# Kernel tuning notes

Measured on AMD Instinct MI355X. Metric: run time of the kernel, lower is better.

The kernel has to match this reference:

```python
import jax, jax.numpy as jnp
import numpy as np

BATCH = 4096
FEAT = 1024
HID = 1024


def setup_inputs() -> dict:
    key = jax.random.key(0)
    ks = jax.random.split(key, 11)
    s_x = 1.0 / np.sqrt(FEAT)
    s_h = 1.0 / np.sqrt(HID)
    return {
        "x": jax.random.normal(ks[0], (BATCH, FEAT), jnp.float32),
        "h_prev": jax.random.normal(ks[1], (BATCH, HID), jnp.float32),
        "c_prev": jax.random.normal(ks[2], (BATCH, HID), jnp.float32),
        # Dense(3*hidden) on x and h (keras Dense: y = x @ W + b)
        "W_ifo_x": jax.random.normal(ks[3], (FEAT, 3 * HID), jnp.float32) * s_x,
        "b_ifo_x": jnp.zeros((3 * HID,), jnp.float32),
        "W_ifo_h": jax.random.normal(ks[4], (HID, 3 * HID), jnp.float32) * s_h,
        "b_ifo_h": jnp.zeros((3 * HID,), jnp.float32),
        # Dense(hidden) on x and h for candidate 'a'
        "W_b_x": jax.random.normal(ks[5], (FEAT, HID), jnp.float32) * s_x,
        "b_b_x": jnp.zeros((HID,), jnp.float32),
        "W_b_h": jax.random.normal(ks[6], (HID, HID), jnp.float32) * s_h,
        "b_b_h": jnp.zeros((HID,), jnp.float32),
    }


def reference(x, h_prev, c_prev, W_ifo_x, b_ifo_x, W_ifo_h, b_ifo_h,
              W_b_x, b_b_x, W_b_h, b_b_h):
    # Fused gate projections: [B, 3H]
    ifo = jax.nn.sigmoid(x @ W_ifo_x + b_ifo_x + h_prev @ W_ifo_h + b_ifo_h)
    i, f, o = jnp.split(ifo, 3, axis=-1)
    a = jnp.tanh(x @ W_b_x + b_b_x + h_prev @ W_b_h + b_b_h)
    c = i * a + f * c_prev
    h = o * jnp.tanh(c)
    return (h, c)
```

## Files before the change

kernel.cpp:

```cpp
#include <hip/hip_runtime.h>
#include <hip/hip_bf16.h>
#include <stdint.h>
#include <stddef.h>


#define BATCH 4096
#define FEAT  1024
#define HID   1024
#define NCAT  4096
#define KCAT  2048

typedef __attribute__((ext_vector_type(8)))  __bf16 bf16x8;
typedef __attribute__((ext_vector_type(16))) float  floatx16;

__device__ __forceinline__ unsigned short f2bf(float f) {
    __hip_bfloat16 b = __float2bfloat16(f);
    return *reinterpret_cast<unsigned short*>(&b);
}
__device__ __forceinline__ void gl2lds16(const unsigned short* g, unsigned short* l) {
    __builtin_amdgcn_global_load_lds(
        (const __attribute__((address_space(1))) void*)g,
        (__attribute__((address_space(3))) void*)l, 16, 0, 0);
}

#define TP_PAD 72
__global__ __launch_bounds__(256)
void pack_all(const float* __restrict__ x, const float* __restrict__ h,
              const float* __restrict__ Wix, const float* __restrict__ Wih,
              const float* __restrict__ Wbx, const float* __restrict__ Wbh,
              unsigned short* __restrict__ Xcat, unsigned short* __restrict__ Wt) {
    __shared__ unsigned short tile[64 * TP_PAD];
    const int t = threadIdx.x;
    const int b = blockIdx.x;
    if (b >= 2048) {
        const int rb = (b - 2048) * 8;
#pragma unroll
        for (int it = 0; it < 8; ++it) {
            const int m = rb + it;
            const float* src = (t < 128) ? (x + (size_t)m * FEAT + t * 8)
                                         : (h + (size_t)m * HID + (t - 128) * 8);
            float4 v0 = *(const float4*)src;
            float4 v1 = *(const float4*)(src + 4);
            union { unsigned short s16[8]; uint4 v; } pk;
            pk.s16[0] = f2bf(v0.x); pk.s16[1] = f2bf(v0.y);
            pk.s16[2] = f2bf(v0.z); pk.s16[3] = f2bf(v0.w);
            pk.s16[4] = f2bf(v1.x); pk.s16[5] = f2bf(v1.y);
            pk.s16[6] = f2bf(v1.z); pk.s16[7] = f2bf(v1.w);
            *(uint4*)(Xcat + (size_t)m * KCAT + t * 8) = pk.v;
        }
        return;
    }
    const int k0 = (b & 31) * 64;
    const int q0 = (b >> 5) * 64;
    const float* src; int stride, cb;
    if (q0 < 3072) { src = (k0 < FEAT) ? Wix : Wih; stride = 3072; cb = q0; }
    else           { src = (k0 < FEAT) ? Wbx : Wbh; stride = 1024; cb = q0 - 3072; }
    const int krow = (k0 < FEAT) ? k0 : (k0 - FEAT);
    {
        int kl = t >> 2;
        int c0 = (t & 3) * 16;
        const float* s = src + (size_t)(krow + kl) * stride + cb + c0;
        union { unsigned short s16[16]; uint4 v[2]; } tmp;
#pragma unroll
        for (int u = 0; u < 16; u += 4) {
            float4 v = *(const float4*)(s + u);
            tmp.s16[u + 0] = f2bf(v.x); tmp.s16[u + 1] = f2bf(v.y);
            tmp.s16[u + 2] = f2bf(v.z); tmp.s16[u + 3] = f2bf(v.w);
        }
        *(uint4*)&tile[kl * TP_PAD + c0]     = tmp.v[0];
        *(uint4*)&tile[kl * TP_PAD + c0 + 8] = tmp.v[1];
    }
    __syncthreads();
    {
        int nl = t >> 2, seg = t & 3;
        int q = q0 + nl;
        int g, j;
        if (q < 3072) { g = q >> 10; j = q & 1023; }
        else          { g = 3;       j = q - 3072; }
        int np = ((j >> 4) << 6) + (g << 4) + (j & 15);
        union { unsigned short s16[16]; uint4 v[2]; } pk;
#pragma unroll
        for (int u = 0; u < 16; ++u)
            pk.s16[u] = tile[(seg * 16 + u) * TP_PAD + nl];
        uint4* dst = (uint4*)(Wt + (size_t)np * KCAT + k0 + seg * 16);
        dst[0] = pk.v[0];
        dst[1] = pk.v[1];
    }
}

#define BM 128
#define BN 128
#define BK 32

__global__ __launch_bounds__(256)
void lstm_fused(const unsigned short* __restrict__ Xcat,
                const unsigned short* __restrict__ Wt,
                const float* __restrict__ c_prev,
                const float* __restrict__ bix, const float* __restrict__ bih,
                const float* __restrict__ bbx, const float* __restrict__ bbh,
                float* __restrict__ out_h, float* __restrict__ out_c) {
    __shared__ unsigned short As[BM * BK];
    __shared__ unsigned short Bs[BN * BK];
    const int t    = threadIdx.x;
    const int lane = t & 63;
    const int wave = t >> 6;
    const int wm   = (wave >> 1) * 64;
    const int wn   = (wave & 1) * 64;

    const int id = blockIdx.x;
    const int grp = id >> 4;
    const int bm = (grp & 7) * 4 + ((id >> 2) & 3);
    const int bn = (grp >> 3) * 4 + (id & 3);
    const int m0 = bm * BM;
    const int n0 = bn * BN;

    floatx16 acc[2][2];
#pragma unroll
    for (int i = 0; i < 2; ++i)
#pragma unroll
        for (int n = 0; n < 2; ++n)
#pragma unroll
            for (int q = 0; q < 16; ++q) acc[i][n][q] = 0.f;

    const int r  = t >> 2;
    const int cA = (((t & 3) ^ ((r >> 1) & 3)) * 8);

    const int rl  = lane & 31;
    const int hi  = lane >> 5;
    const int swz = (rl >> 1) & 3;

    for (int kk = 0; kk < KCAT; kk += BK) {
        __syncthreads();
        gl2lds16(Xcat + (size_t)(m0 + r)      * KCAT + kk + cA, &As[t * 8]);
        gl2lds16(Xcat + (size_t)(m0 + r + 64) * KCAT + kk + cA, &As[t * 8 + 2048]);
        gl2lds16(Wt   + (size_t)(n0 + r)      * KCAT + kk + cA, &Bs[t * 8]);
        gl2lds16(Wt   + (size_t)(n0 + r + 64) * KCAT + kk + cA, &Bs[t * 8 + 2048]);
        __syncthreads();

#pragma unroll
        for (int ks = 0; ks < 2; ++ks) {
            const int co = (((ks * 2 + hi) ^ swz) * 8);
            bf16x8 a0 = *(const bf16x8*)&As[(wm +      rl) * BK + co];
            bf16x8 a1 = *(const bf16x8*)&As[(wm + 32 + rl) * BK + co];
            bf16x8 b0 = *(const bf16x8*)&Bs[(wn +      rl) * BK + co];
            bf16x8 b1 = *(const bf16x8*)&Bs[(wn + 32 + rl) * BK + co];
            acc[0][0] = __builtin_amdgcn_mfma_f32_32x32x16_bf16(a0, b0, acc[0][0], 0, 0, 0);
            acc[0][1] = __builtin_amdgcn_mfma_f32_32x32x16_bf16(a0, b1, acc[0][1], 0, 0, 0);
            acc[1][0] = __builtin_amdgcn_mfma_f32_32x32x16_bf16(a1, b0, acc[1][0], 0, 0, 0);
            acc[1][1] = __builtin_amdgcn_mfma_f32_32x32x16_bf16(a1, b1, acc[1][1], 0, 0, 0);
        }
    }

    const int hl = (lane >> 4) & 1;
    const int jc = lane & 15;
    const int j  = (((n0 + wn) >> 6) << 4) + jc;
    const float bi = bix[j]           + bih[j];
    const float bf = bix[HID + j]     + bih[HID + j];
    const float bo = bix[2 * HID + j] + bih[2 * HID + j];
    const float ba = bbx[j]           + bbh[j];
    const int mbase = m0 + wm + hl * 32 + 4 * hi;
#pragma unroll
    for (int q = 0; q < 4; ++q) {
#pragma unroll
        for (int rr = 0; rr < 4; ++rr) {
            const int reg = q * 4 + rr;
            const int m   = mbase + q * 8 + rr;
            float own0  = hl ? acc[1][0][reg] : acc[0][0][reg];
            float own1  = hl ? acc[1][1][reg] : acc[0][1][reg];
            float send0 = hl ? acc[0][0][reg] : acc[1][0][reg];
            float send1 = hl ? acc[0][1][reg] : acc[1][1][reg];
            float recv0 = __shfl_xor(send0, 16, 64);
            float recv1 = __shfl_xor(send1, 16, 64);
            float gi = (hl ? recv0 : own0) + bi;
            float gf = (hl ? own0 : recv0) + bf;
            float go = (hl ? recv1 : own1) + bo;
            float ga = (hl ? own1 : recv1) + ba;
            float ig = 1.f / (1.f + __expf(-gi));
            float fg = 1.f / (1.f + __expf(-gf));
            float og = 1.f / (1.f + __expf(-go));
            float av = 2.f / (1.f + __expf(-2.f * ga)) - 1.f;
            float cp = c_prev[(size_t)m * HID + j];
            float cv = ig * av + fg * cp;
            float hv = og * (2.f / (1.f + __expf(-2.f * cv)) - 1.f);
            out_h[(size_t)m * HID + j] = hv;
            out_c[(size_t)m * HID + j] = cv;
        }
    }
}

__global__ void naive_lstm(const float* __restrict__ x, const float* __restrict__ h,
                           const float* __restrict__ cvp,
                           const float* __restrict__ Wix, const float* __restrict__ bix,
                           const float* __restrict__ Wih, const float* __restrict__ bih,
                           const float* __restrict__ Wbx, const float* __restrict__ bbx,
                           const float* __restrict__ Wbh, const float* __restrict__ bbh,
                           float* __restrict__ out_h, float* __restrict__ out_c) {
    const int j = blockIdx.x * 256 + threadIdx.x;
    const int m = blockIdx.y;
    float ai = 0.f, af = 0.f, ao = 0.f, aa = 0.f;
    for (int k = 0; k < FEAT; ++k) {
        float xk = x[(size_t)m * FEAT + k];
        ai += xk * Wix[(size_t)k * 3072 + j];
        af += xk * Wix[(size_t)k * 3072 + HID + j];
        ao += xk * Wix[(size_t)k * 3072 + 2 * HID + j];
        aa += xk * Wbx[(size_t)k * HID + j];
    }
    for (int k = 0; k < HID; ++k) {
        float hk = h[(size_t)m * HID + k];
        ai += hk * Wih[(size_t)k * 3072 + j];
        af += hk * Wih[(size_t)k * 3072 + HID + j];
        ao += hk * Wih[(size_t)k * 3072 + 2 * HID + j];
        aa += hk * Wbh[(size_t)k * HID + j];
    }
    ai += bix[j] + bih[j];
    af += bix[HID + j] + bih[HID + j];
    ao += bix[2 * HID + j] + bih[2 * HID + j];
    aa += bbx[j] + bbh[j];
    float ig = 1.f / (1.f + __expf(-ai));
    float fg = 1.f / (1.f + __expf(-af));
    float og = 1.f / (1.f + __expf(-ao));
    float av = 2.f / (1.f + __expf(-2.f * aa)) - 1.f;
    float cp = cvp[(size_t)m * HID + j];
    float cc = ig * av + fg * cp;
    float hh = og * (2.f / (1.f + __expf(-2.f * cc)) - 1.f);
    out_h[(size_t)m * HID + j] = hh;
    out_c[(size_t)m * HID + j] = cc;
}

extern "C" void kernel_launch(void* const* d_in, const int* in_sizes, int n_in,
                              void* d_out, int out_size, void* d_ws, size_t ws_size,
                              hipStream_t stream) {
    const float* x   = (const float*)d_in[0];
    const float* h   = (const float*)d_in[1];
    const float* c   = (const float*)d_in[2];
    const float* Wix = (const float*)d_in[3];
    const float* bix = (const float*)d_in[4];
    const float* Wih = (const float*)d_in[5];
    const float* bih = (const float*)d_in[6];
    const float* Wbx = (const float*)d_in[7];
    const float* bbx = (const float*)d_in[8];
    const float* Wbh = (const float*)d_in[9];
    const float* bbh = (const float*)d_in[10];

    float* out_h = (float*)d_out;
    float* out_c = out_h + (size_t)BATCH * HID;

    const size_t WT_BYTES = (size_t)NCAT * KCAT * 2;
    const size_t XC_BYTES = (size_t)BATCH * KCAT * 2;
    if (ws_size >= WT_BYTES + XC_BYTES) {
        unsigned short* Wt   = (unsigned short*)d_ws;
        unsigned short* Xcat = (unsigned short*)((char*)d_ws + WT_BYTES);
        pack_all<<<2048 + 512, 256, 0, stream>>>(x, h, Wix, Wih, Wbx, Wbh, Xcat, Wt);
        lstm_fused<<<1024, 256, 0, stream>>>(
            Xcat, Wt, c, bix, bih, bbx, bbh, out_h, out_c);
    } else {
        naive_lstm<<<dim3(HID / 256, BATCH), 256, 0, stream>>>(
            x, h, c, Wix, bix, Wih, bih, Wbx, bbx, Wbh, bbh, out_h, out_c);
    }
}
```

Baseline: 234.4 us.

## Double-buffer LDS tiles in fused LSTM GEMM and remap transpose threads

```diff
diff --git a/kernel.cpp b/kernel.cpp
--- a/kernel.cpp
+++ b/kernel.cpp
@@ -72,7 +72,7 @@
     }
     __syncthreads();
     {
-        int nl = t >> 2, seg = t & 3;
+        int seg = t >> 6, nl = t & 63;
         int q = q0 + nl;
         int g, j;
         if (q < 3072) { g = q >> 10; j = q & 1023; }
@@ -99,20 +99,20 @@
                 const float* __restrict__ bix, const float* __restrict__ bih,
                 const float* __restrict__ bbx, const float* __restrict__ bbh,
                 float* __restrict__ out_h, float* __restrict__ out_c) {
-    __shared__ unsigned short As[BM * BK];
-    __shared__ unsigned short Bs[BN * BK];
+    __shared__ unsigned short As[2][BM * BK];
+    __shared__ unsigned short Bs[2][BN * BK];
     const int t    = threadIdx.x;
     const int lane = t & 63;
     const int wave = t >> 6;
     const int wm   = (wave >> 1) * 64;
     const int wn   = (wave & 1) * 64;
 
-    const int id = blockIdx.x;
+    const int id  = blockIdx.x;
     const int grp = id >> 4;
-    const int bm = (grp & 7) * 4 + ((id >> 2) & 3);
-    const int bn = (grp >> 3) * 4 + (id & 3);
-    const int m0 = bm * BM;
-    const int n0 = bn * BN;
+    const int bm  = (grp & 7) * 4 + ((id >> 2) & 3);
+    const int bn  = (grp >> 3) * 4 + (id & 3);
+    const int m0  = bm * BM;
+    const int n0  = bn * BN;
 
     floatx16 acc[2][2];
 #pragma unroll
@@ -129,26 +129,35 @@
     const int hi  = lane >> 5;
     const int swz = (rl >> 1) & 3;
 
+    auto stage = [&](int buf, int kk) {
+        unsigned short* A = &As[buf][0];
+        unsigned short* B = &Bs[buf][0];
+        gl2lds16(Xcat + (size_t)(m0 + r)      * KCAT + kk + cA, &A[t * 8]);
+        gl2lds16(Xcat + (size_t)(m0 + r + 64) * KCAT + kk + cA, &A[t * 8 + 2048]);
+        gl2lds16(Wt   + (size_t)(n0 + r)      * KCAT + kk + cA, &B[t * 8]);
+        gl2lds16(Wt   + (size_t)(n0 + r + 64) * KCAT + kk + cA, &B[t * 8 + 2048]);
+    };
+
+    stage(0, 0);
+    int cur = 0;
     for (int kk = 0; kk < KCAT; kk += BK) {
         __syncthreads();
-        gl2lds16(Xcat + (size_t)(m0 + r)      * KCAT + kk + cA, &As[t * 8]);
-        gl2lds16(Xcat + (size_t)(m0 + r + 64) * KCAT + kk + cA, &As[t * 8 + 2048]);
-        gl2lds16(Wt   + (size_t)(n0 + r)      * KCAT + kk + cA, &Bs[t * 8]);
-        gl2lds16(Wt   + (size_t)(n0 + r + 64) * KCAT + kk + cA, &Bs[t * 8 + 2048]);
-        __syncthreads();
-
+        if (kk + BK < KCAT) stage(cur ^ 1, kk + BK);
+        const unsigned short* A = &As[cur][0];
+        const unsigned short* B = &Bs[cur][0];
 #pragma unroll
         for (int ks = 0; ks < 2; ++ks) {
             const int co = (((ks * 2 + hi) ^ swz) * 8);
-            bf16x8 a0 = *(const bf16x8*)&As[(wm +      rl) * BK + co];
-            bf16x8 a1 = *(const bf16x8*)&As[(wm + 32 + rl) * BK + co];
-            bf16x8 b0 = *(const bf16x8*)&Bs[(wn +      rl) * BK + co];
-            bf16x8 b1 = *(const bf16x8*)&Bs[(wn + 32 + rl) * BK + co];
+            bf16x8 a0 = *(const bf16x8*)&A[(wm +      rl) * BK + co];
+            bf16x8 a1 = *(const bf16x8*)&A[(wm + 32 + rl) * BK + co];
+            bf16x8 b0 = *(const bf16x8*)&B[(wn +      rl) * BK + co];
+            bf16x8 b1 = *(const bf16x8*)&B[(wn + 32 + rl) * BK + co];
             acc[0][0] = __builtin_amdgcn_mfma_f32_32x32x16_bf16(a0, b0, acc[0][0], 0, 0, 0);
             acc[0][1] = __builtin_amdgcn_mfma_f32_32x32x16_bf16(a0, b1, acc[0][1], 0, 0, 0);
             acc[1][0] = __builtin_amdgcn_mfma_f32_32x32x16_bf16(a1, b0, acc[1][0], 0, 0, 0);
             acc[1][1] = __builtin_amdgcn_mfma_f32_32x32x16_bf16(a1, b1, acc[1][1], 0, 0, 0);
         }
+        cur ^= 1;
     }
 
     const int hl = (lane >> 4) & 1;
```

New measurement: 245.5 us. 4.7% more time.
